# Optimization experiments

Hardware: AMD Instinct MI355X
Metric: run time of the kernel (lower is better)

Reference implementation:

```python
import jax, jax.numpy as jnp
import numpy as np

ALPHA = 0.2        # LeakyReLU negative slope
MASK_VAL = -9e15   # matches torch -9000000000000000.0


def setup_inputs() -> dict:
    key = jax.random.key(0)
    k_h, k_adj, k_w, k_a = jax.random.split(key, 4)
    B, N, Nodes, IF, OF = 8, 8, 512, 256, 256
    h = jax.random.normal(k_h, (B, N, Nodes, IF), dtype=jnp.float32)
    adj = jax.random.randint(k_adj, (Nodes, Nodes), 0, 2, dtype=jnp.int32)
    # xavier_uniform with gain=1.414
    gain = 1.414
    lim_w = gain * np.sqrt(6.0 / (IF + OF))
    W = jax.random.uniform(k_w, (IF, OF), dtype=jnp.float32, minval=-lim_w, maxval=lim_w)
    lim_a = gain * np.sqrt(6.0 / (2 * OF + 1))
    a = jax.random.uniform(k_a, (2 * OF, 1), dtype=jnp.float32, minval=-lim_a, maxval=lim_a)
    return {"h": h, "adj": adj, "W": W, "a": a}


def reference(h, adj, W, a):
    # Wh: [B, N, Nodes, OF]
    Wh = jnp.matmul(h, W)
    OF = W.shape[1]
    a1, a2 = a[:OF, 0], a[OF:, 0]
    # e[..., i, j] = leakyrelu(a1 . Wh_i + a2 . Wh_j)  (decomposed additive attention)
    src = jnp.einsum('bnif,f->bni', Wh, a1)  # [B, N, Nodes]
    dst = jnp.einsum('bnjf,f->bnj', Wh, a2)  # [B, N, Nodes]
    e = jax.nn.leaky_relu(src[..., :, None] + dst[..., None, :], negative_slope=ALPHA)
    attention = jnp.where(adj > 0, e, jnp.full_like(e, MASK_VAL))
    attention = jax.nn.softmax(attention, axis=-1)
    # dropout is identity in eval mode (training=False)
    h_prime = jnp.matmul(attention, Wh)  # [B, N, Nodes, OF]
    return jax.nn.elu(h_prime)  # concat=True
```

## Files before the change

kernel.cpp:

```cpp
#include <hip/hip_runtime.h>
#include <hip/hip_bf16.h>


#define ALPHA 0.2f
#define MASK_VAL -9000000000000000.0f
#define NODES 512
#define FDIM 256
#define BN 64

typedef float  f32x4 __attribute__((ext_vector_type(4)));
typedef int    i32x4 __attribute__((ext_vector_type(4)));
typedef short  s16x8 __attribute__((ext_vector_type(8)));
typedef short  s16x4 __attribute__((ext_vector_type(4)));
typedef __bf16 bf16x8 __attribute__((ext_vector_type(8)));

__device__ __forceinline__ unsigned short f2bfu(float x) {
    __hip_bfloat16 b = __float2bfloat16(x);
    unsigned short u; __builtin_memcpy(&u, &b, 2); return u;
}
__device__ __forceinline__ float bfu2f(unsigned short u) {
    unsigned int w = ((unsigned int)u) << 16; return __uint_as_float(w);
}
__device__ __forceinline__ f32x4 mfma16(s16x8 a, s16x8 b, f32x4 c) {
    return __builtin_amdgcn_mfma_f32_16x16x32_bf16(
        __builtin_bit_cast(bf16x8, a), __builtin_bit_cast(bf16x8, b), c, 0, 0, 0);
}

__device__ __forceinline__ void split8v(f32x4 v0, f32x4 v1, s16x8& hi, s16x8& lo)
{
    float x[8] = {v0[0], v0[1], v0[2], v0[3], v1[0], v1[1], v1[2], v1[3]};
    unsigned hw[4], lw[4];
    #pragma unroll
    for (int d = 0; d < 4; ++d) {
        const unsigned u0 = __float_as_uint(x[2*d]);
        const unsigned u1 = __float_as_uint(x[2*d + 1]);
        hw[d] = __builtin_amdgcn_perm(u1, u0, 0x07060302);
        const float l0 = x[2*d]     - __uint_as_float(u0 & 0xFFFF0000u);
        const float l1 = x[2*d + 1] - __uint_as_float(u1 & 0xFFFF0000u);
        lw[d] = __builtin_amdgcn_perm(__float_as_uint(l1), __float_as_uint(l0),
                                      0x07060302);
    }
    hi = __builtin_bit_cast(s16x8, *(unsigned(*)[4])hw);
    lo = __builtin_bit_cast(s16x8, *(unsigned(*)[4])lw);
}

__device__ __forceinline__ void gll16(const void* g, void* l) {
    __builtin_amdgcn_global_load_lds(
        (const __attribute__((address_space(1))) unsigned int*)g,
        (__attribute__((address_space(3))) unsigned int*)l,
        16, 0, 0);
}

__global__ __launch_bounds__(256) void detect_kernel(const unsigned short* __restrict__ hraw,
                                                     int* __restrict__ flag)
{
    const int tid = threadIdx.x;
    float m = 0.0f;
    for (int i = tid; i < 16384; i += 256) {
        unsigned int w = ((unsigned int)hraw[i]) << 16;
        float v = __uint_as_float(w);
        v = fabsf(v);
        if (!(v == v)) v = 1e30f;
        m = fmaxf(m, v);
    }
    #pragma unroll
    for (int off = 32; off >= 1; off >>= 1)
        m = fmaxf(m, __shfl_down(m, off));
    __shared__ float red[4];
    if ((tid & 63) == 0) red[tid >> 6] = m;
    __syncthreads();
    if (tid == 0) {
        float mm = fmaxf(fmaxf(red[0], red[1]), fmaxf(red[2], red[3]));
        *flag = (mm > 1e4f) ? 1 : 0;
    }
}

__global__ __launch_bounds__(256) void prep_w_kernel(
    const void* __restrict__ Wv, const int* __restrict__ flagp,
    short* __restrict__ WtHi, short* __restrict__ WtLo)
{
    const int flag = *flagp;
    __shared__ float tile[16][17];
    const int tx = threadIdx.x & 15, ty = threadIdx.x >> 4;
    const int kk = blockIdx.y * 16 + ty;
    const int f  = blockIdx.x * 16 + tx;
    float v;
    if (flag) v = ((const float*)Wv)[kk * FDIM + f];
    else      v = bfu2f(((const unsigned short*)Wv)[kk * FDIM + f]);
    tile[ty][tx] = v;
    __syncthreads();
    const float x = tile[tx][ty];
    const int fo = blockIdx.x * 16 + ty;
    const int ko = blockIdx.y * 16 + tx;
    unsigned short h = f2bfu(x);
    WtHi[fo * FDIM + ko] = (short)h;
    WtLo[fo * FDIM + ko] = (short)f2bfu(x - bfu2f(h));
}

__global__ __launch_bounds__(256, 2) void wh_gemm(
    const void* __restrict__ hv,
    const short* __restrict__ WtHi, const short* __restrict__ WtLo,
    const void* __restrict__ av, const int* __restrict__ flagp,
    short* __restrict__ WhTHi, short* __restrict__ WhTLo,
    float* __restrict__ srcv, float* __restrict__ dstv)
{
    __shared__ __align__(16) char smem[67584];

    const int flag = *flagp;
    const int blk = blockIdx.x;
    const int bn  = blk >> 3;
    const int i0  = (blk & 7) * 64;
    const size_t r0g = (size_t)blk * 64;
    const int tid = threadIdx.x;
    const int w = tid >> 6, l = tid & 63;
    const int fb = l & 15, g = l >> 4;

    if (flag) {
        const int srow = tid >> 2, q = tid & 3;
        const float* gA = (const float*)hv + (r0g + srow) * FDIM;
        #pragma unroll
        for (int i = 0; i < 8; ++i) {
            const int seg = q + 4 * i;
            f32x4 v0 = *(const f32x4*)(gA + seg * 8);
            f32x4 v1 = *(const f32x4*)(gA + seg * 8 + 4);
            s16x8 hi, lo; split8v(v0, v1, hi, lo);
            const int slot = seg ^ (srow & 7);
            *(s16x8*)(smem + srow * 512 + slot * 16) = hi;
            *(s16x8*)(smem + 32768 + srow * 512 + slot * 16) = lo;
        }
    } else {
        const short* hs = (const short*)hv;
        const unsigned wub = (unsigned)(tid & ~63);
        #pragma unroll
        for (int i = 0; i < 8; ++i) {
            const int idx = i * 256 + tid;
            const int row = idx >> 5, slot = idx & 31;
            const int srcseg = slot ^ (row & 7);
            gll16(hs + (r0g + row) * FDIM + srcseg * 8,
                  smem + (i * 256 + (int)wub) * 16);
        }
    }
    __syncthreads();

    f32x4 acc[4][4];
    #pragma unroll
    for (int rt = 0; rt < 4; ++rt)
        #pragma unroll
        for (int ct = 0; ct < 4; ++ct) acc[rt][ct] = f32x4{0.f,0.f,0.f,0.f};

    if (flag) {
        #pragma unroll
        for (int t = 0; t < 8; ++t) {
            s16x8 bh[4], bl[4], ah[4], al[4];
            #pragma unroll
            for (int ct = 0; ct < 4; ++ct) {
                const int f = w * 64 + ct * 16 + fb;
                bh[ct] = *(const s16x8*)(WtHi + f * FDIM + t * 32 + g * 8);
                bl[ct] = *(const s16x8*)(WtLo + f * FDIM + t * 32 + g * 8);
            }
            #pragma unroll
            for (int rt = 0; rt < 4; ++rt) {
                const int row = rt * 16 + fb;
                const int slot = (t * 4 + g) ^ (row & 7);
                ah[rt] = *(const s16x8*)(smem + row * 512 + slot * 16);
                al[rt] = *(const s16x8*)(smem + 32768 + row * 512 + slot * 16);
            }
            #pragma unroll
            for (int rt = 0; rt < 4; ++rt)
                #pragma unroll
                for (int ct = 0; ct < 4; ++ct) {
                    acc[rt][ct] = mfma16(ah[rt], bh[ct], acc[rt][ct]);
                    acc[rt][ct] = mfma16(al[rt], bh[ct], acc[rt][ct]);
                    acc[rt][ct] = mfma16(ah[rt], bl[ct], acc[rt][ct]);
                }
        }
    } else {
        #pragma unroll
        for (int t = 0; t < 8; ++t) {
            s16x8 bh[4], ah[4];
            #pragma unroll
            for (int ct = 0; ct < 4; ++ct) {
                const int f = w * 64 + ct * 16 + fb;
                bh[ct] = *(const s16x8*)(WtHi + f * FDIM + t * 32 + g * 8);
            }
            #pragma unroll
            for (int rt = 0; rt < 4; ++rt) {
                const int row = rt * 16 + fb;
                const int slot = (t * 4 + g) ^ (row & 7);
                ah[rt] = *(const s16x8*)(smem + row * 512 + slot * 16);
            }
            #pragma unroll
            for (int rt = 0; rt < 4; ++rt)
                #pragma unroll
                for (int ct = 0; ct < 4; ++ct)
                    acc[rt][ct] = mfma16(ah[rt], bh[ct], acc[rt][ct]);
        }
    }

    const size_t wbT = (size_t)bn * FDIM * NODES;
    #pragma unroll
    for (int rt = 0; rt < 4; ++rt) {
        const int orow = i0 + rt * 16 + g * 4;
        #pragma unroll
        for (int ct = 0; ct < 4; ++ct) {
            const int f = w * 64 + ct * 16 + fb;
            s16x4 h4, l4;
            #pragma unroll
            for (int r = 0; r < 4; ++r) {
                float x = acc[rt][ct][r];
                unsigned short hh = f2bfu(x);
                h4[r] = (short)hh;
                l4[r] = (short)f2bfu(x - bfu2f(hh));
            }
            *(s16x4*)(WhTHi + wbT + (size_t)f * NODES + orow) = h4;
            *(s16x4*)(WhTLo + wbT + (size_t)f * NODES + orow) = l4;
        }
    }

    float a1v[4], a2v[4];
    #pragma unroll
    for (int ct = 0; ct < 4; ++ct) {
        const int f = w * 64 + ct * 16 + fb;
        if (flag) {
            a1v[ct] = ((const float*)av)[f];
            a2v[ct] = ((const float*)av)[FDIM + f];
        } else {
            a1v[ct] = bfu2f(((const unsigned short*)av)[f]);
            a2v[ct] = bfu2f(((const unsigned short*)av)[FDIM + f]);
        }
    }
    float* red1 = (float*)(smem + 65536);
    float* red2 = red1 + 256;
    #pragma unroll
    for (int rt = 0; rt < 4; ++rt) {
        #pragma unroll
        for (int r = 0; r < 4; ++r) {
            float s1 = 0.f, s2 = 0.f;
            #pragma unroll
            for (int ct = 0; ct < 4; ++ct) {
                s1 = fmaf(acc[rt][ct][r], a1v[ct], s1);
                s2 = fmaf(acc[rt][ct][r], a2v[ct], s2);
            }
            #pragma unroll
            for (int off = 1; off <= 8; off <<= 1) {
                s1 += __shfl_xor(s1, off);
                s2 += __shfl_xor(s2, off);
            }
            if (fb == 0) {
                red1[w * 64 + rt * 16 + g * 4 + r] = s1;
                red2[w * 64 + rt * 16 + g * 4 + r] = s2;
            }
        }
    }
    __syncthreads();
    if (tid < 64) {
        srcv[bn * NODES + i0 + tid] =
            red1[tid] + red1[64 + tid] + red1[128 + tid] + red1[192 + tid];
        dstv[bn * NODES + i0 + tid] =
            red2[tid] + red2[64 + tid] + red2[128 + tid] + red2[192 + tid];
    }
}

__global__ __launch_bounds__(512, 4) void pv_gemm(
    const short* __restrict__ WhTHi, const short* __restrict__ WhTLo,
    const float* __restrict__ srcv, const float* __restrict__ dstv,
    const int* __restrict__ adj, const int* __restrict__ flagp,
    void* __restrict__ out)
{
    __shared__ __align__(16) char smem[65792];

    const int flag = *flagp;
    const int b0 = blockIdx.x;
    const int blk = (b0 & 7) * 64 + (b0 >> 3);
    const int bn  = blk >> 3;
    const int i0  = (blk & 7) * 64;
    const int tid = threadIdx.x;
    const int w = tid >> 6, l = tid & 63;

    const short* bhig = WhTHi + (size_t)bn * FDIM * NODES;
    const short* blog = WhTLo + (size_t)bn * FDIM * NODES;
    float* rowinvS = (float*)(smem + 65536);

    {
        const float* drow = dstv + bn * NODES;
        const int j = l * 8;
        for (int rr = 0; rr < 8; ++rr) {
            const int r = w * 8 + rr;
            const int* adjrow = adj + (size_t)(i0 + r) * NODES;
            const float srow = srcv[bn * NODES + i0 + r];
            const i32x4 q0 = *(const i32x4*)(adjrow + j);
            const i32x4 q1 = *(const i32x4*)(adjrow + j + 4);
            const f32x4 d0 = *(const f32x4*)(drow + j);
            const f32x4 d1 = *(const f32x4*)(drow + j + 4);
            float e[8];
            #pragma unroll
            for (int k = 0; k < 4; ++k) {
                float ev = srow + d0[k];
                ev = (ev > 0.f) ? ev : ALPHA * ev;
                e[k] = (q0[k] > 0) ? ev : MASK_VAL;
                float ew = srow + d1[k];
                ew = (ew > 0.f) ? ew : ALPHA * ew;
                e[4 + k] = (q1[k] > 0) ? ew : MASK_VAL;
            }
            float m = e[0];
            #pragma unroll
            for (int k = 1; k < 8; ++k) m = fmaxf(m, e[k]);
            #pragma unroll
            for (int off = 1; off <= 32; off <<= 1) m = fmaxf(m, __shfl_xor(m, off));
            float p[8], s = 0.f;
            #pragma unroll
            for (int k = 0; k < 8; ++k) {
                p[k] = __expf(e[k] - m);
                s += p[k];
            }
            #pragma unroll
            for (int off = 1; off <= 32; off <<= 1) s += __shfl_xor(s, off);
            const float isum = 1.0f / s;
            s16x8 ph;
            #pragma unroll
            for (int k = 0; k < 8; ++k) ph[k] = (short)f2bfu(p[k] * isum);
            *(s16x8*)(smem + r * 1024 + ((l ^ (r & 7)) * 16)) = ph;
            if (l == 0) rowinvS[r] = isum;
        }
    }
    __syncthreads();

    const int fb = l & 15, g = l >> 4;
    const int f0 = w * 32 + fb;
    const int f1 = f0 + 16;
    const short* gH0 = bhig + (size_t)f0 * NODES + g * 8;
    const short* gH1 = bhig + (size_t)f1 * NODES + g * 8;
    const short* gL0 = blog + (size_t)f0 * NODES + g * 8;
    const short* gL1 = blog + (size_t)f1 * NODES + g * 8;

    f32x4 acc[4][2];
    #pragma unroll
    for (int rt = 0; rt < 4; ++rt)
        #pragma unroll
        for (int ct = 0; ct < 2; ++ct) acc[rt][ct] = f32x4{0.f,0.f,0.f,0.f};

    #pragma unroll 4
    for (int t = 0; t < 16; ++t) {
        s16x8 bh0 = *(const s16x8*)(gH0 + t * 32);
        s16x8 bh1 = *(const s16x8*)(gH1 + t * 32);
        s16x8 bl0 = *(const s16x8*)(gL0 + t * 32);
        s16x8 bl1 = *(const s16x8*)(gL1 + t * 32);
        s16x8 af[4];
        #pragma unroll
        for (int rt = 0; rt < 4; ++rt) {
            const int row = rt * 16 + fb;
            const unsigned seg = (unsigned)(t * 4 + g) ^ (unsigned)(row & 7);
            af[rt] = *(const s16x8*)(smem + (unsigned)(row * 1024) + seg * 16);
        }
        #pragma unroll
        for (int rt = 0; rt < 4; ++rt) {
            acc[rt][0] = mfma16(af[rt], bh0, acc[rt][0]);
            acc[rt][0] = mfma16(af[rt], bl0, acc[rt][0]);
            acc[rt][1] = mfma16(af[rt], bh1, acc[rt][1]);
            acc[rt][1] = mfma16(af[rt], bl1, acc[rt][1]);
        }
    }

    #pragma unroll
    for (int rt = 0; rt < 4; ++rt) {
        #pragma unroll
        for (int ct = 0; ct < 2; ++ct) {
            const int f = w * 32 + ct * 16 + fb;
            #pragma unroll
            for (int r = 0; r < 4; ++r) {
                float v = acc[rt][ct][r];
                v = (v > 0.f) ? v : expm1f(v);
                const size_t o = ((size_t)bn * NODES + i0 + rt * 16 + g * 4 + r) * FDIM + f;
                if (flag) ((float*)out)[o] = v;
                else      ((unsigned short*)out)[o] = f2bfu(v);
            }
        }
    }
}

extern "C" void kernel_launch(void* const* d_in, const int* in_sizes, int n_in,
                              void* d_out, int out_size, void* d_ws, size_t ws_size,
                              hipStream_t stream)
{
    const void* h   = d_in[0];
    const int*  adj = (const int*)d_in[1];
    const void* W   = d_in[2];
    const void* a   = d_in[3];

    int*   flag  = (int*)d_ws;
    float* srcv  = (float*)d_ws + 64;
    float* dstv  = srcv + BN * NODES;
    short* WtHi  = (short*)(dstv + BN * NODES);
    short* WtLo  = WtHi + FDIM * FDIM;
    short* WhTHi = WtLo + FDIM * FDIM;
    short* WhTLo = WhTHi + (size_t)BN * FDIM * NODES;

    detect_kernel<<<1, 256, 0, stream>>>((const unsigned short*)h, flag);
    prep_w_kernel<<<dim3(16, 16), 256, 0, stream>>>(W, flag, WtHi, WtLo);
    wh_gemm<<<512, 256, 0, stream>>>(h, WtHi, WtLo, a, flag,
                                     WhTHi, WhTLo, srcv, dstv);
    pv_gemm<<<512, 512, 0, stream>>>(WhTHi, WhTLo, srcv, dstv, adj, flag, d_out);
}
```

Measured before the change: 169.9 us.

## Double wh_gemm block width and software-pipeline B-operand loads in both GEMMs

wh_gemm now launches 512 threads per block, with each of 8 waves covering 32 output features instead of 64, which halves accumulator registers per wave. The reduction buffers are resized to hold 8 partial sums. Both GEMMs now prefetch global B-fragments two K-steps ahead through a 3-slot register ring and raise wave priority around the MFMA bursts, aiming to hide global load latency. The unused rowinvS shared buffer in pv_gemm is dropped. Costs include more waves per block and higher prefetch register pressure, and the launch bound of 4 blocks of 512 threads may not be reachable given about 68KB of shared memory per block.

```diff
diff --git a/kernel.cpp b/kernel.cpp
--- a/kernel.cpp
+++ b/kernel.cpp
@@ -97,14 +97,14 @@
     WtLo[fo * FDIM + ko] = (short)f2bfu(x - bfu2f(h));
 }
 
-__global__ __launch_bounds__(256, 2) void wh_gemm(
+__global__ __launch_bounds__(512, 4) void wh_gemm(
     const void* __restrict__ hv,
     const short* __restrict__ WtHi, const short* __restrict__ WtLo,
     const void* __restrict__ av, const int* __restrict__ flagp,
     short* __restrict__ WhTHi, short* __restrict__ WhTLo,
     float* __restrict__ srcv, float* __restrict__ dstv)
 {
-    __shared__ __align__(16) char smem[67584];
+    __shared__ __align__(16) char smem[69632];
 
     const int flag = *flagp;
     const int blk = blockIdx.x;
@@ -116,11 +116,11 @@
     const int fb = l & 15, g = l >> 4;
 
     if (flag) {
-        const int srow = tid >> 2, q = tid & 3;
+        const int srow = tid >> 3, q = tid & 7;
         const float* gA = (const float*)hv + (r0g + srow) * FDIM;
         #pragma unroll
-        for (int i = 0; i < 8; ++i) {
-            const int seg = q + 4 * i;
+        for (int i = 0; i < 4; ++i) {
+            const int seg = q + 8 * i;
             f32x4 v0 = *(const f32x4*)(gA + seg * 8);
             f32x4 v1 = *(const f32x4*)(gA + seg * 8 + 4);
             s16x8 hi, lo; split8v(v0, v1, hi, lo);
@@ -132,32 +132,49 @@
         const short* hs = (const short*)hv;
         const unsigned wub = (unsigned)(tid & ~63);
         #pragma unroll
-        for (int i = 0; i < 8; ++i) {
-            const int idx = i * 256 + tid;
+        for (int i = 0; i < 4; ++i) {
+            const int idx = i * 512 + tid;
             const int row = idx >> 5, slot = idx & 31;
             const int srcseg = slot ^ (row & 7);
             gll16(hs + (r0g + row) * FDIM + srcseg * 8,
-                  smem + (i * 256 + (int)wub) * 16);
+                  smem + (i * 512 + (int)wub) * 16);
         }
     }
     __syncthreads();
 
-    f32x4 acc[4][4];
+    f32x4 acc[4][2];
     #pragma unroll
     for (int rt = 0; rt < 4; ++rt)
         #pragma unroll
-        for (int ct = 0; ct < 4; ++ct) acc[rt][ct] = f32x4{0.f,0.f,0.f,0.f};
+        for (int ct = 0; ct < 2; ++ct) acc[rt][ct] = f32x4{0.f,0.f,0.f,0.f};
+
+    const int f0 = w * 32 + fb;
+    const int f1 = f0 + 16;
+    const short* gH0 = WtHi + f0 * FDIM + g * 8;
+    const short* gH1 = WtHi + f1 * FDIM + g * 8;
+    const short* gL0 = WtLo + f0 * FDIM + g * 8;
+    const short* gL1 = WtLo + f1 * FDIM + g * 8;
 
     if (flag) {
+        s16x8 pb[3][4];
+        #pragma unroll
+        for (int d = 0; d < 2; ++d) {
+            pb[d][0] = *(const s16x8*)(gH0 + d * 32);
+            pb[d][1] = *(const s16x8*)(gH1 + d * 32);
+            pb[d][2] = *(const s16x8*)(gL0 + d * 32);
+            pb[d][3] = *(const s16x8*)(gL1 + d * 32);
+        }
         #pragma unroll
         for (int t = 0; t < 8; ++t) {
-            s16x8 bh[4], bl[4], ah[4], al[4];
-            #pragma unroll
-            for (int ct = 0; ct < 4; ++ct) {
-                const int f = w * 64 + ct * 16 + fb;
-                bh[ct] = *(const s16x8*)(WtHi + f * FDIM + t * 32 + g * 8);
-                bl[ct] = *(const s16x8*)(WtLo + f * FDIM + t * 32 + g * 8);
-            }
+            const int cur = t % 3;
+            if (t + 2 < 8) {
+                const int nx = (t + 2) % 3;
+                pb[nx][0] = *(const s16x8*)(gH0 + (t + 2) * 32);
+                pb[nx][1] = *(const s16x8*)(gH1 + (t + 2) * 32);
+                pb[nx][2] = *(const s16x8*)(gL0 + (t + 2) * 32);
+                pb[nx][3] = *(const s16x8*)(gL1 + (t + 2) * 32);
+            }
+            s16x8 ah[4], al[4];
             #pragma unroll
             for (int rt = 0; rt < 4; ++rt) {
                 const int row = rt * 16 + fb;
@@ -165,35 +182,47 @@
                 ah[rt] = *(const s16x8*)(smem + row * 512 + slot * 16);
                 al[rt] = *(const s16x8*)(smem + 32768 + row * 512 + slot * 16);
             }
-            #pragma unroll
-            for (int rt = 0; rt < 4; ++rt)
-                #pragma unroll
-                for (int ct = 0; ct < 4; ++ct) {
-                    acc[rt][ct] = mfma16(ah[rt], bh[ct], acc[rt][ct]);
-                    acc[rt][ct] = mfma16(al[rt], bh[ct], acc[rt][ct]);
-                    acc[rt][ct] = mfma16(ah[rt], bl[ct], acc[rt][ct]);
-                }
+            __builtin_amdgcn_s_setprio(1);
+            #pragma unroll
+            for (int rt = 0; rt < 4; ++rt) {
+                acc[rt][0] = mfma16(ah[rt], pb[cur][0], acc[rt][0]);
+                acc[rt][0] = mfma16(al[rt], pb[cur][0], acc[rt][0]);
+                acc[rt][0] = mfma16(ah[rt], pb[cur][2], acc[rt][0]);
+                acc[rt][1] = mfma16(ah[rt], pb[cur][1], acc[rt][1]);
+                acc[rt][1] = mfma16(al[rt], pb[cur][1], acc[rt][1]);
+                acc[rt][1] = mfma16(ah[rt], pb[cur][3], acc[rt][1]);
+            }
+            __builtin_amdgcn_s_setprio(0);
         }
     } else {
+        s16x8 pb[3][2];
+        #pragma unroll
+        for (int d = 0; d < 2; ++d) {
+            pb[d][0] = *(const s16x8*)(gH0 + d * 32);
+            pb[d][1] = *(const s16x8*)(gH1 + d * 32);
+        }
         #pragma unroll
         for (int t = 0; t < 8; ++t) {
-            s16x8 bh[4], ah[4];
-            #pragma unroll
-            for (int ct = 0; ct < 4; ++ct) {
-                const int f = w * 64 + ct * 16 + fb;
-                bh[ct] = *(const s16x8*)(WtHi + f * FDIM + t * 32 + g * 8);
-            }
+            const int cur = t % 3;
+            if (t + 2 < 8) {
+                const int nx = (t + 2) % 3;
+                pb[nx][0] = *(const s16x8*)(gH0 + (t + 2) * 32);
+                pb[nx][1] = *(const s16x8*)(gH1 + (t + 2) * 32);
+            }
+            s16x8 ah[4];
             #pragma unroll
             for (int rt = 0; rt < 4; ++rt) {
                 const int row = rt * 16 + fb;
                 const int slot = (t * 4 + g) ^ (row & 7);
                 ah[rt] = *(const s16x8*)(smem + row * 512 + slot * 16);
             }
-            #pragma unroll
-            for (int rt = 0; rt < 4; ++rt)
-                #pragma unroll
-                for (int ct = 0; ct < 4; ++ct)
-                    acc[rt][ct] = mfma16(ah[rt], bh[ct], acc[rt][ct]);
+            __builtin_amdgcn_s_setprio(1);
+            #pragma unroll
+            for (int rt = 0; rt < 4; ++rt) {
+                acc[rt][0] = mfma16(ah[rt], pb[cur][0], acc[rt][0]);
+                acc[rt][1] = mfma16(ah[rt], pb[cur][1], acc[rt][1]);
+            }
+            __builtin_amdgcn_s_setprio(0);
         }
     }
 
@@ -202,8 +231,8 @@
     for (int rt = 0; rt < 4; ++rt) {
         const int orow = i0 + rt * 16 + g * 4;
         #pragma unroll
-        for (int ct = 0; ct < 4; ++ct) {
-            const int f = w * 64 + ct * 16 + fb;
+        for (int ct = 0; ct < 2; ++ct) {
+            const int f = w * 32 + ct * 16 + fb;
             s16x4 h4, l4;
             #pragma unroll
             for (int r = 0; r < 4; ++r) {
@@ -217,10 +246,10 @@
         }
     }
 
-    float a1v[4], a2v[4];
-    #pragma unroll
-    for (int ct = 0; ct < 4; ++ct) {
-        const int f = w * 64 + ct * 16 + fb;
+    float a1v[2], a2v[2];
+    #pragma unroll
+    for (int ct = 0; ct < 2; ++ct) {
+        const int f = w * 32 + ct * 16 + fb;
         if (flag) {
             a1v[ct] = ((const float*)av)[f];
             a2v[ct] = ((const float*)av)[FDIM + f];
@@ -230,14 +259,14 @@
         }
     }
     float* red1 = (float*)(smem + 65536);
-    float* red2 = red1 + 256;
+    float* red2 = (float*)(smem + 67584);
     #pragma unroll
     for (int rt = 0; rt < 4; ++rt) {
         #pragma unroll
         for (int r = 0; r < 4; ++r) {
             float s1 = 0.f, s2 = 0.f;
             #pragma unroll
-            for (int ct = 0; ct < 4; ++ct) {
+            for (int ct = 0; ct < 2; ++ct) {
                 s1 = fmaf(acc[rt][ct][r], a1v[ct], s1);
                 s2 = fmaf(acc[rt][ct][r], a2v[ct], s2);
             }
@@ -254,10 +283,14 @@
     }
     __syncthreads();
     if (tid < 64) {
-        srcv[bn * NODES + i0 + tid] =
-            red1[tid] + red1[64 + tid] + red1[128 + tid] + red1[192 + tid];
-        dstv[bn * NODES + i0 + tid] =
-            red2[tid] + red2[64 + tid] + red2[128 + tid] + red2[192 + tid];
+        float s1 = 0.f, s2 = 0.f;
+        #pragma unroll
+        for (int ww = 0; ww < 8; ++ww) {
+            s1 += red1[ww * 64 + tid];
+            s2 += red2[ww * 64 + tid];
+        }
+        srcv[bn * NODES + i0 + tid] = s1;
+        dstv[bn * NODES + i0 + tid] = s2;
     }
 }
 
@@ -267,7 +300,7 @@
     const int* __restrict__ adj, const int* __restrict__ flagp,
     void* __restrict__ out)
 {
-    __shared__ __align__(16) char smem[65792];
+    __shared__ __align__(16) char smem[65536];
 
     const int flag = *flagp;
     const int b0 = blockIdx.x;
@@ -279,7 +312,6 @@
 
     const short* bhig = WhTHi + (size_t)bn * FDIM * NODES;
     const short* blog = WhTLo + (size_t)bn * FDIM * NODES;
-    float* rowinvS = (float*)(smem + 65536);
 
     {
         const float* drow = dstv + bn * NODES;
@@ -320,7 +352,6 @@
             #pragma unroll
             for (int k = 0; k < 8; ++k) ph[k] = (short)f2bfu(p[k] * isum);
             *(s16x8*)(smem + r * 1024 + ((l ^ (r & 7)) * 16)) = ph;
-            if (l == 0) rowinvS[r] = isum;
         }
     }
     __syncthreads();
@@ -339,12 +370,24 @@
         #pragma unroll
         for (int ct = 0; ct < 2; ++ct) acc[rt][ct] = f32x4{0.f,0.f,0.f,0.f};
 
-    #pragma unroll 4
+    s16x8 pb[3][4];
+    #pragma unroll
+    for (int d = 0; d < 2; ++d) {
+        pb[d][0] = *(const s16x8*)(gH0 + d * 32);
+        pb[d][1] = *(const s16x8*)(gH1 + d * 32);
+        pb[d][2] = *(const s16x8*)(gL0 + d * 32);
+        pb[d][3] = *(const s16x8*)(gL1 + d * 32);
+    }
+    #pragma unroll
     for (int t = 0; t < 16; ++t) {
-        s16x8 bh0 = *(const s16x8*)(gH0 + t * 32);
-        s16x8 bh1 = *(const s16x8*)(gH1 + t * 32);
-        s16x8 bl0 = *(const s16x8*)(gL0 + t * 32);
-        s16x8 bl1 = *(const s16x8*)(gL1 + t * 32);
+        const int cur = t % 3;
+        if (t + 2 < 16) {
+            const int nx = (t + 2) % 3;
+            pb[nx][0] = *(const s16x8*)(gH0 + (t + 2) * 32);
+            pb[nx][1] = *(const s16x8*)(gH1 + (t + 2) * 32);
+            pb[nx][2] = *(const s16x8*)(gL0 + (t + 2) * 32);
+            pb[nx][3] = *(const s16x8*)(gL1 + (t + 2) * 32);
+        }
         s16x8 af[4];
         #pragma unroll
         for (int rt = 0; rt < 4; ++rt) {
@@ -352,13 +395,15 @@
             const unsigned seg = (unsigned)(t * 4 + g) ^ (unsigned)(row & 7);
             af[rt] = *(const s16x8*)(smem + (unsigned)(row * 1024) + seg * 16);
         }
+        __builtin_amdgcn_s_setprio(1);
         #pragma unroll
         for (int rt = 0; rt < 4; ++rt) {
-            acc[rt][0] = mfma16(af[rt], bh0, acc[rt][0]);
-            acc[rt][0] = mfma16(af[rt], bl0, acc[rt][0]);
-            acc[rt][1] = mfma16(af[rt], bh1, acc[rt][1]);
-            acc[rt][1] = mfma16(af[rt], bl1, acc[rt][1]);
-        }
+            acc[rt][0] = mfma16(af[rt], pb[cur][0], acc[rt][0]);
+            acc[rt][0] = mfma16(af[rt], pb[cur][2], acc[rt][0]);
+            acc[rt][1] = mfma16(af[rt], pb[cur][1], acc[rt][1]);
+            acc[rt][1] = mfma16(af[rt], pb[cur][3], acc[rt][1]);
+        }
+        __builtin_amdgcn_s_setprio(0);
     }
 
     #pragma unroll
@@ -397,7 +442,7 @@
 
     detect_kernel<<<1, 256, 0, stream>>>((const unsigned short*)h, flag);
     prep_w_kernel<<<dim3(16, 16), 256, 0, stream>>>(W, flag, WtHi, WtLo);
-    wh_gemm<<<512, 256, 0, stream>>>(h, WtHi, WtLo, a, flag,
+    wh_gemm<<<512, 512, 0, stream>>>(h, WtHi, WtLo, a, flag,
                                      WhTHi, WhTLo, srcv, dstv);
     pv_gemm<<<512, 512, 0, stream>>>(WhTHi, WhTLo, srcv, dstv, adj, flag, d_out);
 }
```

Measured after the change: 167.4 us. About the same (-1.5%).
